# Kernel optimization log

Measured on AMD Instinct MI355X. Metric: run time of the kernel, lower is better.

## Reference

```python
import jax, jax.numpy as jnp
import numpy as np
import math

B, S, D, H = 2, 2048, 2048, 16
HD = D // H  # head_dim = 128
NEG = -9e15


def setup_inputs() -> dict:
    key = jax.random.key(0)
    k1, k2, k3 = jax.random.split(key, 3)
    x = jax.random.normal(k1, (B, S, D), dtype=jnp.float32)
    Wqkv = jax.random.normal(k2, (D, 3 * D), dtype=jnp.float32) * (1.0 / math.sqrt(D))
    bqkv = jnp.zeros((3 * D,), dtype=jnp.float32)
    Wo = jax.random.normal(k3, (D, D), dtype=jnp.float32) * (1.0 / math.sqrt(D))
    bo = jnp.zeros((D,), dtype=jnp.float32)
    return {"x": x, "Wqkv": Wqkv, "bqkv": bqkv, "Wo": Wo, "bo": bo}


def reference(x, Wqkv, bqkv, Wo, bo):
    b, s, d = x.shape
    # fused QKV projection
    qkv = x @ Wqkv + bqkv                       # [B,S,3D]
    qkv = qkv.reshape(b, s, H, 3 * HD)          # per-head interleaved q|k|v
    qkv = qkv.transpose(0, 2, 1, 3)             # [B,H,S,3*HD]
    q, k, v = jnp.split(qkv, 3, axis=-1)        # each [B,H,S,HD]
    scale = 1.0 / math.sqrt(HD)
    logits = jnp.einsum('bhqd,bhkd->bhqk', q, k) * scale  # [B,H,S,S]
    causal = jnp.tril(jnp.ones((s, s), dtype=bool))[None, None]
    logits = jnp.where(causal, logits, NEG)
    score = jax.nn.softmax(logits, axis=-1)
    attn = jnp.einsum('bhqk,bhkd->bhqd', score, v)         # [B,H,S,HD]
    attn = attn.transpose(0, 2, 1, 3).reshape(b, s, d)
    return attn @ Wo + bo
```

## Files before the change

kernel.cpp:

```cpp
#include <hip/hip_runtime.h>
#include <stdint.h>

#define DEV static __device__ __forceinline__

typedef _Float16 half8 __attribute__((ext_vector_type(8)));
typedef _Float16 half4 __attribute__((ext_vector_type(4)));
typedef float f32x4 __attribute__((ext_vector_type(4)));
typedef uint16_t u16x8 __attribute__((ext_vector_type(8)));

constexpr int Bc = 2, Sc = 2048, Dc = 2048, Hc = 16, HDc = 128;
constexpr int D3c = 3 * Dc;
constexpr int Mc = Bc * Sc;

DEV void gl_lds16(const void* g, void* l) {
    __builtin_amdgcn_global_load_lds(
        (const __attribute__((address_space(1))) unsigned int*)g,
        (__attribute__((address_space(3))) unsigned int*)l,
        16, 0, 0);
}

DEV void transpose_tile(const float* __restrict__ in, _Float16* __restrict__ out,
                        int R, int C, int bx, int by, int t)
{
    __shared__ float ls[64][64];
    const int r0 = by * 64, c0 = bx * 64;
    {
        const int rr = t >> 4, lc = t & 15;
#pragma unroll
        for (int p = 0; p < 4; ++p) {
            int r = p * 16 + rr;
            int pc = lc ^ ((r >> 3) & 7);
            *(float4*)&ls[r][pc * 4] =
                *(const float4*)&in[(size_t)(r0 + r) * C + c0 + lc * 4];
        }
    }
    __syncthreads();
    {
        const int oc = t >> 3, ss = (t & 7) * 8;
#pragma unroll
        for (int p = 0; p < 2; ++p) {
            int c = p * 32 + oc;
            int lc = c >> 2, wi = c & 3;
            half8 hv;
#pragma unroll
            for (int j = 0; j < 8; ++j) {
                int r = ss + j;
                hv[j] = (_Float16)ls[r][(lc ^ ((r >> 3) & 7)) * 4 + wi];
            }
            *(half8*)&out[(size_t)(c0 + c) * R + r0 + ss] = hv;
        }
    }
}

__global__ __launch_bounds__(256) void prep_kernel(
    const float* __restrict__ x, const float* __restrict__ Wqkv,
    const float* __restrict__ Wo,
    _Float16* __restrict__ xb, _Float16* __restrict__ wt1,
    _Float16* __restrict__ wt2)
{
    const int id = blockIdx.x, t = threadIdx.x;
    if (id < 4096) {
        int i = id * 256 + t;
        const float4* p = (const float4*)x;
        float4 a = p[i * 2], b = p[i * 2 + 1];
        half8 hv;
        hv[0] = (_Float16)a.x; hv[1] = (_Float16)a.y; hv[2] = (_Float16)a.z; hv[3] = (_Float16)a.w;
        hv[4] = (_Float16)b.x; hv[5] = (_Float16)b.y; hv[6] = (_Float16)b.z; hv[7] = (_Float16)b.w;
        *(half8*)(xb + (size_t)i * 8) = hv;
    } else if (id < 4096 + 3072) {
        int id2 = id - 4096;
        transpose_tile(Wqkv, wt1, Dc, D3c, id2 % 96, id2 / 96, t);
    } else {
        int id3 = id - 7168;
        transpose_tile(Wo, wt2, Dc, Dc, id3 & 31, id3 >> 5, t);
    }
}

__global__ __launch_bounds__(256) void transpose_v_kernel(
    const uint16_t* __restrict__ qkv, uint16_t* __restrict__ vt)
{
    __shared__ uint16_t ls[64][64];
    const int t = threadIdx.x;
    const int s0 = blockIdx.x * 64, d0 = blockIdx.y * 64, bh = blockIdx.z;
    const int b = bh >> 4, h = bh & 15;
    {
        const int sr = t >> 3, lc = t & 7;
#pragma unroll
        for (int p = 0; p < 2; ++p) {
            int s = p * 32 + sr;
            int pc = lc ^ ((s >> 3) & 7);
            *(u16x8*)&ls[s][pc * 8] =
                *(const u16x8*)&qkv[(size_t)(b * Sc + s0 + s) * D3c + h * 384 + 256 + d0 + lc * 8];
        }
    }
    __syncthreads();
    {
        const int od = t >> 3, ss = (t & 7) * 8;
#pragma unroll
        for (int p = 0; p < 2; ++p) {
            int d = p * 32 + od;
            int lc = d >> 3, wi = d & 7;
            u16x8 hv;
#pragma unroll
            for (int j = 0; j < 8; ++j) {
                int s = ss + j;
                hv[j] = ls[s][(lc ^ ((s >> 3) & 7)) * 8 + wi];
            }
            *(u16x8*)&vt[(size_t)(bh * HDc + d0 + d) * Sc + s0 + ss] = hv;
        }
    }
}

template <int BF16OUT>
__global__ __launch_bounds__(256, 2) void gemm_bt_kernel(
    const _Float16* __restrict__ A, const _Float16* __restrict__ Bt,
    const float* __restrict__ bias, void* __restrict__ Cout,
    int M, int N, int K)
{
    __shared__ __align__(16) char smem[32768];
    char* sA = smem;
    char* sB = smem + 16384;
    const int t = threadIdx.x, w = t >> 6, lane = t & 63;
    const int quad = lane >> 4, l15 = lane & 15;
    const int wr = w >> 1, wc = w & 1;
    const int n0 = blockIdx.x * 128, m0 = blockIdx.y * 128;

    const f32x4 vzero = {0.f, 0.f, 0.f, 0.f};
    f32x4 acc[4][4];
#pragma unroll
    for (int i = 0; i < 4; ++i)
#pragma unroll
        for (int j = 0; j < 4; ++j) acc[i][j] = vzero;

    const int kiters = K >> 6;
    for (int kk = 0; kk < kiters; ++kk) {
#pragma unroll
        for (int i = 0; i < 4; ++i) {
            int c = i * 256 + t;
            int row = c >> 3, kbs = c & 7, kact = kbs ^ (row & 7);
            gl_lds16(A + (size_t)(m0 + row) * K + kk * 64 + kact * 8,
                     sA + (i * 256 + w * 64) * 16);
        }
#pragma unroll
        for (int i = 0; i < 4; ++i) {
            int c = i * 256 + t;
            int row = c >> 3, kbs = c & 7, kact = kbs ^ (row & 7);
            gl_lds16(Bt + (size_t)(n0 + row) * K + kk * 64 + kact * 8,
                     sB + (i * 256 + w * 64) * 16);
        }
        __syncthreads();
#pragma unroll
        for (int ks = 0; ks < 2; ++ks) {
            half8 af[4], bf[4];
#pragma unroll
            for (int mt = 0; mt < 4; ++mt) {
                int row = wr * 64 + mt * 16 + l15;
                int kact = (ks * 4 + quad) ^ (l15 & 7);
                af[mt] = *(const half8*)(sA + row * 128 + kact * 16);
            }
#pragma unroll
            for (int nt = 0; nt < 4; ++nt) {
                int row = wc * 64 + nt * 16 + l15;
                int kact = (ks * 4 + quad) ^ (l15 & 7);
                bf[nt] = *(const half8*)(sB + row * 128 + kact * 16);
            }
#pragma unroll
            for (int mt = 0; mt < 4; ++mt)
#pragma unroll
                for (int nt = 0; nt < 4; ++nt)
                    acc[mt][nt] = __builtin_amdgcn_mfma_f32_16x16x32_f16(
                        af[mt], bf[nt], acc[mt][nt], 0, 0, 0);
        }
        __syncthreads();
    }

#pragma unroll
    for (int nt = 0; nt < 4; ++nt) {
        int col = n0 + wc * 64 + nt * 16 + l15;
        float bv = bias[col];
#pragma unroll
        for (int mt = 0; mt < 4; ++mt)
#pragma unroll
            for (int r = 0; r < 4; ++r) {
                int row = m0 + wr * 64 + mt * 16 + quad * 4 + r;
                float v = acc[mt][nt][r] + bv;
                if (BF16OUT) ((_Float16*)Cout)[(size_t)row * N + col] = (_Float16)v;
                else         ((float*)Cout)[(size_t)row * N + col] = v;
            }
    }
}

__global__ __launch_bounds__(512, 4) void flash_kernel(
    const _Float16* __restrict__ qkv, const _Float16* __restrict__ vt,
    _Float16* __restrict__ attn)
{
    __shared__ __align__(16) char smem[65536];
    char* sKc = smem;            char* sVc = smem + 16384;
    char* sKn = smem + 32768;    char* sVn = smem + 49152;

    const int t = threadIdx.x, w = t >> 6, lane = t & 63;
    const int quad = lane >> 4, l15 = lane & 15;
    const int bh = blockIdx.x;
    const int by = blockIdx.y;
    const int qt = (by < 8) ? 15 - by : by - 8;
    const int b = bh >> 4, h = bh & 15;
    const int q0 = qt * 128;
    const int qrow = q0 + w * 16 + l15;

    half8 qf[4];
#pragma unroll
    for (int ks = 0; ks < 4; ++ks) {
        const _Float16* p = qkv + (size_t)(b * Sc + qrow) * D3c +
                            h * 384 + ks * 32 + quad * 8;
        qf[ks] = *(const half8*)p;
    }

    const f32x4 vzero = {0.f, 0.f, 0.f, 0.f};
    f32x4 o[8];
#pragma unroll
    for (int dt = 0; dt < 8; ++dt) o[dt] = vzero;
    float m_st = -1e30f, l_st = 0.f;

    const float kScale = 0.08838834764831845f * 1.4426950408889634f;
    const int nkt = 2 * qt + 2;

    auto stageKV = [&](char* sK, char* sV, int kt) {
#pragma unroll
        for (int i = 0; i < 2; ++i) {
            int c = i * 512 + t;
            int row = c >> 4, kbs = c & 15, kact = kbs ^ (row & 15);
            gl_lds16(qkv + (size_t)(b * Sc + kt * 64 + row) * D3c + h * 384 + 128 + kact * 8,
                     sK + (i * 512 + w * 64) * 16);
        }
#pragma unroll
        for (int i = 0; i < 2; ++i) {
            int c = i * 512 + t;
            int row = c >> 3, kbs = c & 7, kact = kbs ^ (row & 7);
            gl_lds16(vt + (size_t)(bh * HDc + row) * Sc + kt * 64 + kact * 8,
                     sV + (i * 512 + w * 64) * 16);
        }
    };

    stageKV(sKc, sVc, 0);
    __syncthreads();

    for (int kt = 0; kt < nkt; ++kt) {
        if (kt + 1 < nkt) stageKV(sKn, sVn, kt + 1);

        f32x4 sf[4];
#pragma unroll
        for (int kb = 0; kb < 4; ++kb) sf[kb] = vzero;
#pragma unroll
        for (int ks = 0; ks < 4; ++ks) {
#pragma unroll
            for (int kb = 0; kb < 4; ++kb) {
                int row = kb * 16 + l15;
                int slot = (ks * 4 + quad) ^ l15;
                half8 kf = *(const half8*)(sKc + row * 256 + slot * 16);
                sf[kb] = __builtin_amdgcn_mfma_f32_16x16x32_f16(kf, qf[ks], sf[kb], 0, 0, 0);
            }
        }

        const bool domask = (kt >= 2 * qt);
        float rm = -1e30f;
#pragma unroll
        for (int kb = 0; kb < 4; ++kb)
#pragma unroll
            for (int r = 0; r < 4; ++r) {
                float v = sf[kb][r] * kScale;
                if (domask) {
                    int col = kt * 64 + kb * 16 + quad * 4 + r;
                    if (col > qrow) v = -1e30f;
                }
                sf[kb][r] = v;
                rm = fmaxf(rm, v);
            }
        rm = fmaxf(rm, __shfl_xor(rm, 16, 64));
        rm = fmaxf(rm, __shfl_xor(rm, 32, 64));
        float mn = fmaxf(m_st, rm);
        float alpha = __builtin_amdgcn_exp2f(m_st - mn);
        m_st = mn;

        half4 pb[4];
        float rs = 0.f;
#pragma unroll
        for (int kb = 0; kb < 4; ++kb)
#pragma unroll
            for (int r = 0; r < 4; ++r) {
                float p = __builtin_amdgcn_exp2f(sf[kb][r] - mn);
                rs += p;
                pb[kb][r] = (_Float16)p;
            }
        rs += __shfl_xor(rs, 16, 64);
        rs += __shfl_xor(rs, 32, 64);
        l_st = l_st * alpha + rs;

#pragma unroll
        for (int dt = 0; dt < 8; ++dt)
#pragma unroll
            for (int r = 0; r < 4; ++r) o[dt][r] *= alpha;

#pragma unroll
        for (int kb = 0; kb < 4; ++kb) {
#pragma unroll
            for (int dt = 0; dt < 8; ++dt) {
                int row = dt * 16 + l15;
                int slot = (kb * 2 + (quad >> 1)) ^ (l15 & 7);
                half4 vf = *(const half4*)(sVc + row * 128 + slot * 16 + (quad & 1) * 8);
                o[dt] = __builtin_amdgcn_mfma_f32_16x16x16f16(vf, pb[kb], o[dt], 0, 0, 0);
            }
        }

        __syncthreads();
        char* tp;
        tp = sKc; sKc = sKn; sKn = tp;
        tp = sVc; sVc = sVn; sVn = tp;
    }

    char* sO = smem;
    float linv = 1.0f / l_st;
#pragma unroll
    for (int dt = 0; dt < 8; ++dt) {
        half4 hv;
#pragma unroll
        for (int r = 0; r < 4; ++r) hv[r] = (_Float16)(o[dt][r] * linv);
        *(half4*)(sO + (w * 16 + l15) * 272 + (dt * 16 + quad * 4) * 2) = hv;
    }
    __syncthreads();
#pragma unroll
    for (int i = 0; i < 4; ++i) {
        int q = i * 32 + (t >> 4);
        int d = (t & 15) * 8;
        half8 hv = *(const half8*)(sO + q * 272 + d * 2);
        *(half8*)(attn + (size_t)(b * Sc + q0 + q) * Dc + h * HDc + d) = hv;
    }
}

extern "C" void kernel_launch(void* const* d_in, const int* in_sizes, int n_in,
                              void* d_out, int out_size, void* d_ws, size_t ws_size,
                              hipStream_t stream)
{
    (void)in_sizes; (void)n_in; (void)out_size; (void)ws_size;
    const float* x    = (const float*)d_in[0];
    const float* Wqkv = (const float*)d_in[1];
    const float* bqkv = (const float*)d_in[2];
    const float* Wo   = (const float*)d_in[3];
    const float* bo   = (const float*)d_in[4];
    float* out = (float*)d_out;

    _Float16* xb  = (_Float16*)d_ws;
    _Float16* wt1 = xb  + (size_t)Mc * Dc;
    _Float16* wt2 = wt1 + (size_t)D3c * Dc;
    _Float16* qkv = wt2 + (size_t)Dc * Dc;
    _Float16* vtg  = wt1;
    _Float16* attn = xb;

    prep_kernel<<<8192, 256, 0, stream>>>(x, Wqkv, Wo, xb, wt1, wt2);
    gemm_bt_kernel<1><<<dim3(D3c / 128, Mc / 128), 256, 0, stream>>>(
        xb, wt1, bqkv, qkv, Mc, D3c, Dc);
    transpose_v_kernel<<<dim3(Sc / 64, 2, Bc * Hc), 256, 0, stream>>>(
        (const uint16_t*)qkv, (uint16_t*)vtg);
    flash_kernel<<<dim3(Bc * Hc, 16), 512, 0, stream>>>(qkv, vtg, attn);
    gemm_bt_kernel<0><<<dim3(Dc / 128, Mc / 128), 256, 0, stream>>>(
        attn, wt2, bo, out, Mc, Dc, Dc);
}
```

Baseline: 360.9 us.

## Give each flash-attention wave two 16-row query groups and halve block threads

The flash kernel now runs 4 waves of 256 threads instead of 8 waves of 512. Each wave processes 32 query rows as two 16-row groups, so every K and V fragment read from LDS feeds two MFMAs. This cuts LDS read traffic per MFMA and keeps the tile at 128 queries. In exchange, register pressure roughly doubles for the accumulators and there are fewer waves per block to hide latency, with launch bounds lowered to match.

```diff
diff --git a/kernel.cpp b/kernel.cpp
--- a/kernel.cpp
+++ b/kernel.cpp
@@ -190,7 +190,7 @@
     }
 }
 
-__global__ __launch_bounds__(512, 4) void flash_kernel(
+__global__ __launch_bounds__(256, 2) void flash_kernel(
     const _Float16* __restrict__ qkv, const _Float16* __restrict__ vt,
     _Float16* __restrict__ attn)
 {
@@ -205,39 +205,43 @@
     const int qt = (by < 8) ? 15 - by : by - 8;
     const int b = bh >> 4, h = bh & 15;
     const int q0 = qt * 128;
-    const int qrow = q0 + w * 16 + l15;
-
-    half8 qf[4];
-#pragma unroll
-    for (int ks = 0; ks < 4; ++ks) {
-        const _Float16* p = qkv + (size_t)(b * Sc + qrow) * D3c +
-                            h * 384 + ks * 32 + quad * 8;
-        qf[ks] = *(const half8*)p;
-    }
+    const int qbase = q0 + w * 32 + l15;
+
+    half8 qf[2][4];
+#pragma unroll
+    for (int g = 0; g < 2; ++g)
+#pragma unroll
+        for (int ks = 0; ks < 4; ++ks) {
+            const _Float16* p = qkv + (size_t)(b * Sc + qbase + g * 16) * D3c +
+                                h * 384 + ks * 32 + quad * 8;
+            qf[g][ks] = *(const half8*)p;
+        }
 
     const f32x4 vzero = {0.f, 0.f, 0.f, 0.f};
-    f32x4 o[8];
-#pragma unroll
-    for (int dt = 0; dt < 8; ++dt) o[dt] = vzero;
-    float m_st = -1e30f, l_st = 0.f;
+    f32x4 o[2][8];
+#pragma unroll
+    for (int g = 0; g < 2; ++g)
+#pragma unroll
+        for (int dt = 0; dt < 8; ++dt) o[g][dt] = vzero;
+    float m_st[2] = {-1e30f, -1e30f}, l_st[2] = {0.f, 0.f};
 
     const float kScale = 0.08838834764831845f * 1.4426950408889634f;
     const int nkt = 2 * qt + 2;
 
     auto stageKV = [&](char* sK, char* sV, int kt) {
 #pragma unroll
-        for (int i = 0; i < 2; ++i) {
-            int c = i * 512 + t;
+        for (int i = 0; i < 4; ++i) {
+            int c = i * 256 + t;
             int row = c >> 4, kbs = c & 15, kact = kbs ^ (row & 15);
             gl_lds16(qkv + (size_t)(b * Sc + kt * 64 + row) * D3c + h * 384 + 128 + kact * 8,
-                     sK + (i * 512 + w * 64) * 16);
-        }
-#pragma unroll
-        for (int i = 0; i < 2; ++i) {
-            int c = i * 512 + t;
+                     sK + (i * 256 + w * 64) * 16);
+        }
+#pragma unroll
+        for (int i = 0; i < 4; ++i) {
+            int c = i * 256 + t;
             int row = c >> 3, kbs = c & 7, kact = kbs ^ (row & 7);
             gl_lds16(vt + (size_t)(bh * HDc + row) * Sc + kt * 64 + kact * 8,
-                     sV + (i * 512 + w * 64) * 16);
+                     sV + (i * 256 + w * 64) * 16);
         }
     };
 
@@ -247,9 +251,11 @@
     for (int kt = 0; kt < nkt; ++kt) {
         if (kt + 1 < nkt) stageKV(sKn, sVn, kt + 1);
 
-        f32x4 sf[4];
-#pragma unroll
-        for (int kb = 0; kb < 4; ++kb) sf[kb] = vzero;
+        f32x4 sf[2][4];
+#pragma unroll
+        for (int g = 0; g < 2; ++g)
+#pragma unroll
+            for (int kb = 0; kb < 4; ++kb) sf[g][kb] = vzero;
 #pragma unroll
         for (int ks = 0; ks < 4; ++ks) {
 #pragma unroll
@@ -257,48 +263,53 @@
                 int row = kb * 16 + l15;
                 int slot = (ks * 4 + quad) ^ l15;
                 half8 kf = *(const half8*)(sKc + row * 256 + slot * 16);
-                sf[kb] = __builtin_amdgcn_mfma_f32_16x16x32_f16(kf, qf[ks], sf[kb], 0, 0, 0);
+                sf[0][kb] = __builtin_amdgcn_mfma_f32_16x16x32_f16(kf, qf[0][ks], sf[0][kb], 0, 0, 0);
+                sf[1][kb] = __builtin_amdgcn_mfma_f32_16x16x32_f16(kf, qf[1][ks], sf[1][kb], 0, 0, 0);
             }
         }
 
         const bool domask = (kt >= 2 * qt);
-        float rm = -1e30f;
-#pragma unroll
-        for (int kb = 0; kb < 4; ++kb)
-#pragma unroll
-            for (int r = 0; r < 4; ++r) {
-                float v = sf[kb][r] * kScale;
-                if (domask) {
-                    int col = kt * 64 + kb * 16 + quad * 4 + r;
-                    if (col > qrow) v = -1e30f;
+        half4 pb[2][4];
+#pragma unroll
+        for (int g = 0; g < 2; ++g) {
+            const int qr = qbase + g * 16;
+            float rm = -1e30f;
+#pragma unroll
+            for (int kb = 0; kb < 4; ++kb)
+#pragma unroll
+                for (int r = 0; r < 4; ++r) {
+                    float v = sf[g][kb][r] * kScale;
+                    if (domask) {
+                        int col = kt * 64 + kb * 16 + quad * 4 + r;
+                        if (col > qr) v = -1e30f;
+                    }
+                    sf[g][kb][r] = v;
+                    rm = fmaxf(rm, v);
                 }
-                sf[kb][r] = v;
-                rm = fmaxf(rm, v);
-            }
-        rm = fmaxf(rm, __shfl_xor(rm, 16, 64));
-        rm = fmaxf(rm, __shfl_xor(rm, 32, 64));
-        float mn = fmaxf(m_st, rm);
-        float alpha = __builtin_amdgcn_exp2f(m_st - mn);
-        m_st = mn;
-
-        half4 pb[4];
-        float rs = 0.f;
-#pragma unroll
-        for (int kb = 0; kb < 4; ++kb)
-#pragma unroll
-            for (int r = 0; r < 4; ++r) {
-                float p = __builtin_amdgcn_exp2f(sf[kb][r] - mn);
-                rs += p;
-                pb[kb][r] = (_Float16)p;
-            }
-        rs += __shfl_xor(rs, 16, 64);
-        rs += __shfl_xor(rs, 32, 64);
-        l_st = l_st * alpha + rs;
-
-#pragma unroll
-        for (int dt = 0; dt < 8; ++dt)
-#pragma unroll
-            for (int r = 0; r < 4; ++r) o[dt][r] *= alpha;
+            rm = fmaxf(rm, __shfl_xor(rm, 16, 64));
+            rm = fmaxf(rm, __shfl_xor(rm, 32, 64));
+            float mn = fmaxf(m_st[g], rm);
+            float alpha = __builtin_amdgcn_exp2f(m_st[g] - mn);
+            m_st[g] = mn;
+
+            float rs = 0.f;
+#pragma unroll
+            for (int kb = 0; kb < 4; ++kb)
+#pragma unroll
+                for (int r = 0; r < 4; ++r) {
+                    float p = __builtin_amdgcn_exp2f(sf[g][kb][r] - mn);
+                    rs += p;
+                    pb[g][kb][r] = (_Float16)p;
+                }
+            rs += __shfl_xor(rs, 16, 64);
+            rs += __shfl_xor(rs, 32, 64);
+            l_st[g] = l_st[g] * alpha + rs;
+
+#pragma unroll
+            for (int dt = 0; dt < 8; ++dt)
+#pragma unroll
+                for (int r = 0; r < 4; ++r) o[g][dt][r] *= alpha;
+        }
 
 #pragma unroll
         for (int kb = 0; kb < 4; ++kb) {
@@ -307,7 +318,8 @@
                 int row = dt * 16 + l15;
                 int slot = (kb * 2 + (quad >> 1)) ^ (l15 & 7);
                 half4 vf = *(const half4*)(sVc + row * 128 + slot * 16 + (quad & 1) * 8);
-                o[dt] = __builtin_amdgcn_mfma_f32_16x16x16f16(vf, pb[kb], o[dt], 0, 0, 0);
+                o[0][dt] = __builtin_amdgcn_mfma_f32_16x16x16f16(vf, pb[0][kb], o[0][dt], 0, 0, 0);
+                o[1][dt] = __builtin_amdgcn_mfma_f32_16x16x16f16(vf, pb[1][kb], o[1][dt], 0, 0, 0);
             }
         }
 
@@ -318,18 +330,21 @@
     }
 
     char* sO = smem;
-    float linv = 1.0f / l_st;
-#pragma unroll
-    for (int dt = 0; dt < 8; ++dt) {
-        half4 hv;
-#pragma unroll
-        for (int r = 0; r < 4; ++r) hv[r] = (_Float16)(o[dt][r] * linv);
-        *(half4*)(sO + (w * 16 + l15) * 272 + (dt * 16 + quad * 4) * 2) = hv;
+#pragma unroll
+    for (int g = 0; g < 2; ++g) {
+        float linv = 1.0f / l_st[g];
+#pragma unroll
+        for (int dt = 0; dt < 8; ++dt) {
+            half4 hv;
+#pragma unroll
+            for (int r = 0; r < 4; ++r) hv[r] = (_Float16)(o[g][dt][r] * linv);
+            *(half4*)(sO + (w * 32 + g * 16 + l15) * 272 + (dt * 16 + quad * 4) * 2) = hv;
+        }
     }
     __syncthreads();
 #pragma unroll
-    for (int i = 0; i < 4; ++i) {
-        int q = i * 32 + (t >> 4);
+    for (int i = 0; i < 8; ++i) {
+        int q = i * 16 + (t >> 4);
         int d = (t & 15) * 8;
         half8 hv = *(const half8*)(sO + q * 272 + d * 2);
         *(half8*)(attn + (size_t)(b * Sc + q0 + q) * Dc + h * HDc + d) = hv;
@@ -360,7 +375,7 @@
         xb, wt1, bqkv, qkv, Mc, D3c, Dc);
     transpose_v_kernel<<<dim3(Sc / 64, 2, Bc * Hc), 256, 0, stream>>>(
         (const uint16_t*)qkv, (uint16_t*)vtg);
-    flash_kernel<<<dim3(Bc * Hc, 16), 512, 0, stream>>>(qkv, vtg, attn);
+    flash_kernel<<<dim3(Bc * Hc, 16), 256, 0, stream>>>(qkv, vtg, attn);
     gemm_bt_kernel<0><<<dim3(Dc / 128, Mc / 128), 256, 0, stream>>>(
         attn, wt2, bo, out, Mc, Dc, Dc);
 }
```

Result: slower. 369.1 us (+2.3%).
